# Performance work log

Measured on AMD Instinct MI355X. Metric: run time of the kernel, lower is better.

Reference implementation:

```python
import jax, jax.numpy as jnp
import numpy as np

B, N, D, H = 32, 512, 768, 12
HD = D // H  # 64
EPS = 1e-5


def layer_norm(x, g, b):
    mu = jnp.mean(x, axis=-1, keepdims=True)
    var = jnp.mean((x - mu) ** 2, axis=-1, keepdims=True)
    return (x - mu) / jnp.sqrt(var + EPS) * g + b


def setup_inputs() -> dict:
    key = jax.random.key(0)
    ks = jax.random.split(key, 10)
    x = jax.random.normal(ks[0], (B, N, D), dtype=jnp.float32)
    adj = jax.random.randint(ks[1], (B, N, N), 0, 2).astype(jnp.int32)
    adj = jnp.maximum(adj, jnp.eye(N, dtype=jnp.int32)[None])  # self-loops
    init = lambda k, shape: (jax.random.normal(k, shape, dtype=jnp.float32) * 0.02)
    return {
        "x": x, "adj": adj,
        "wq": init(ks[2], (D, D)), "bq": jnp.zeros((D,), jnp.float32),
        "wk": init(ks[3], (D, D)), "bk": jnp.zeros((D,), jnp.float32),
        "wv": init(ks[4], (D, D)), "bv": jnp.zeros((D,), jnp.float32),
        "wo": init(ks[5], (D, D)), "bo": jnp.zeros((D,), jnp.float32),
        "g1": jnp.ones((D,), jnp.float32), "b1": jnp.zeros((D,), jnp.float32),
        "g2": jnp.ones((D,), jnp.float32), "b2": jnp.zeros((D,), jnp.float32),
        "w_ffn1": init(ks[6], (D, 4 * D)), "b_ffn1": jnp.zeros((4 * D,), jnp.float32),
        "w_ffn2": init(ks[7], (4 * D, D)), "b_ffn2": jnp.zeros((D,), jnp.float32),
    }


def reference(x, adj, wq, bq, wk, bk, wv, bv, wo, bo, g1, b1, g2, b2,
              w_ffn1, b_ffn1, w_ffn2, b_ffn2):
    scale = HD ** -0.5
    h = layer_norm(x, g1, b1)
    split = lambda t: t.reshape(B, N, H, HD).transpose(0, 2, 1, 3)  # [B,H,N,HD]
    q = split(h @ wq + bq)
    k = split(h @ wk + bk)
    v = split(h @ wv + bv)
    scores = jnp.einsum('bhnd,bhmd->bhnm', q, k) * scale  # [B,H,N,N]
    scores = jnp.where(adj[:, None, :, :] == 0, -jnp.inf, scores)
    attn = jax.nn.softmax(scores, axis=-1)
    attn = jnp.nan_to_num(attn, nan=0.0)  # rows with no edges -> 0
    out = jnp.einsum('bhnm,bhmd->bhnd', attn, v)
    out = out.transpose(0, 2, 1, 3).reshape(B, N, D)
    out = out @ wo + bo + x  # residual (dropout=0, eval mode)
    h2 = layer_norm(out, g2, b2)
    ffn = jax.nn.gelu(h2 @ w_ffn1 + b_ffn1, approximate=False) @ w_ffn2 + b_ffn2
    return out + ffn
```

## Files before the change

kernel.cpp:

```cpp
#include <hip/hip_runtime.h>


#define Bn 32
#define Nn 512
#define Dn 768
#define Hn 12
#define HDn 64
#define Mn (Bn * Nn)
#define DFn 3072
#define MCHUNK 8192

typedef unsigned short u16;
typedef unsigned long long u64;
typedef short bf16x8 __attribute__((ext_vector_type(8)));
typedef float f32x4 __attribute__((ext_vector_type(4)));
typedef unsigned short u16x8 __attribute__((ext_vector_type(8)));

__device__ __forceinline__ float b2f(u16 u) {
    return __uint_as_float(((unsigned int)u) << 16);
}
__device__ __forceinline__ u16 f2b(float f) {
    unsigned int u = __float_as_uint(f);
    u += 0x7fffu + ((u >> 16) & 1u);
    return (u16)(u >> 16);
}
__device__ __forceinline__ float loadDyn(const void* p, size_t i, int f) {
    return f ? ((const float*)p)[i] : b2f(((const u16*)p)[i]);
}
__device__ __forceinline__ float gelu_exact(float x) {
    return 0.5f * x * (1.0f + erff(x * 0.70710678118654752f));
}

__device__ __forceinline__ void gl_lds16(const u16* g, u16* l) {
    __builtin_amdgcn_global_load_lds(
        (const __attribute__((address_space(1))) void*)(unsigned long long)(const void*)g,
        (__attribute__((address_space(3))) void*)(unsigned)(unsigned long long)(void*)l,
        16, 0, 0);
}

__global__ __launch_bounds__(256) void sniff_k(const u16* __restrict__ x,
                                               int* __restrict__ flag) {
    const int idx = blockIdx.x * 256 + threadIdx.x;
    u16x8 a = *(const u16x8*)&x[(size_t)idx * 8];
    int cnt = 0;
#pragma unroll
    for (int e = 0; e < 8; e++)
        cnt += ((a[e] & 0x7F80) == 0x7F80) ? 1 : 0;
#pragma unroll
    for (int off = 1; off <= 32; off <<= 1) cnt += __shfl_xor(cnt, off, 64);
    if ((threadIdx.x & 63) == 0 && cnt > 0) atomicAdd(flag, cnt);
}

__device__ __forceinline__ int flagval(const int* flagp) {
    return (*flagp > 32) ? 1 : 0;
}

__global__ __launch_bounds__(256) void pack_bias_k(
    const void* __restrict__ bq, const void* __restrict__ bk,
    const void* __restrict__ bv, const void* __restrict__ bo,
    const void* __restrict__ bf1, const void* __restrict__ bf2,
    float* __restrict__ out, const int* __restrict__ flagp) {
    const int f = flagval(flagp);
    const int i = blockIdx.x * 256 + threadIdx.x;
    if (i >= 6912) return;
    const void* src;
    int off;
    if (i < 768)       { src = bq;  off = i; }
    else if (i < 1536) { src = bk;  off = i - 768; }
    else if (i < 2304) { src = bv;  off = i - 1536; }
    else if (i < 3072) { src = bo;  off = i - 2304; }
    else if (i < 6144) { src = bf1; off = i - 3072; }
    else               { src = bf2; off = i - 6144; }
    out[i] = loadDyn(src, off, f);
}

__global__ __launch_bounds__(256) void mask_build_k(
    const int* __restrict__ adj, u64* __restrict__ mask) {
    const int idx = blockIdx.x * 256 + threadIdx.x;
    const size_t base = (size_t)(idx >> 3) * Nn + (size_t)(idx & 7) * 64;
    const int4* p = (const int4*)(adj + base);
    u64 m = 0;
#pragma unroll
    for (int c = 0; c < 16; c++) {
        int4 a = p[c];
        if (a.x) m |= 1ull << (c * 4 + 0);
        if (a.y) m |= 1ull << (c * 4 + 1);
        if (a.z) m |= 1ull << (c * 4 + 2);
        if (a.w) m |= 1ull << (c * 4 + 3);
    }
    mask[idx] = m;
}

__global__ __launch_bounds__(256) void transpose_k(
    const void* __restrict__ in, u16* __restrict__ out, int R, int C,
    const int* __restrict__ flagp) {
    const int f = flagval(flagp);
    __shared__ u16 tile[32][33];
    int c0 = blockIdx.x * 32, r0 = blockIdx.y * 32;
    int tx = threadIdx.x, ty = threadIdx.y;
#pragma unroll
    for (int i = 0; i < 32; i += 8)
        tile[ty + i][tx] = f2b(loadDyn(in, (size_t)(r0 + ty + i) * C + c0 + tx, f));
    __syncthreads();
#pragma unroll
    for (int i = 0; i < 32; i += 8)
        out[(size_t)(c0 + ty + i) * R + r0 + tx] = tile[tx][ty + i];
}

__global__ __launch_bounds__(256) void vtrans_k(
    const u16* __restrict__ v, u16* __restrict__ vt) {
    __shared__ u16 tile[32][33];
    const int bh = blockIdx.z;
    const int d0 = blockIdx.x * 32;
    const int n0 = blockIdx.y * 32;
    const int b = bh / Hn, h = bh % Hn;
    const int tx = threadIdx.x, ty = threadIdx.y;
#pragma unroll
    for (int i = 0; i < 32; i += 8)
        tile[ty + i][tx] =
            v[(size_t)(b * Nn + n0 + ty + i) * Dn + h * HDn + d0 + tx];
    __syncthreads();
#pragma unroll
    for (int i = 0; i < 32; i += 8)
        vt[((size_t)bh * HDn + d0 + ty + i) * Nn + n0 + tx] = tile[tx][ty + i];
}

template <int XDYN>
__global__ __launch_bounds__(256) void ln_k(
    const void* __restrict__ x, const void* __restrict__ g,
    const void* __restrict__ b, u16* __restrict__ y,
    const int* __restrict__ flagp) {
    const int f = flagval(flagp);
    const int t = threadIdx.x;
    const int row = blockIdx.x * 8 + (t >> 5);
    const int l32 = t & 31;
    const size_t base = (size_t)row * Dn;
    float v[24];
    if (XDYN == 0 || f == 0) {
        const u16* xp = (const u16*)x;
#pragma unroll
        for (int kk = 0; kk < 3; kk++) {
            u16x8 a = *(const u16x8*)&xp[base + kk * 256 + l32 * 8];
#pragma unroll
            for (int e = 0; e < 8; e++) v[kk * 8 + e] = b2f(a[e]);
        }
    } else {
#pragma unroll
        for (int kk = 0; kk < 3; kk++)
#pragma unroll
            for (int e = 0; e < 8; e++)
                v[kk * 8 + e] = loadDyn(x, base + kk * 256 + l32 * 8 + e, f);
    }
    float s = 0.f;
#pragma unroll
    for (int i = 0; i < 24; i++) s += v[i];
#pragma unroll
    for (int off = 1; off <= 16; off <<= 1) s += __shfl_xor(s, off, 64);
    const float mu = s * (1.0f / Dn);
    float d2 = 0.f;
#pragma unroll
    for (int i = 0; i < 24; i++) { float d = v[i] - mu; d2 += d * d; }
#pragma unroll
    for (int off = 1; off <= 16; off <<= 1) d2 += __shfl_xor(d2, off, 64);
    const float rstd = rsqrtf(d2 * (1.0f / Dn) + 1e-5f);
#pragma unroll
    for (int kk = 0; kk < 3; kk++) {
        const int c0 = kk * 256 + l32 * 8;
        u16x8 o;
        if (f == 0) {
            u16x8 gv = *(const u16x8*)&((const u16*)g)[c0];
            u16x8 bv = *(const u16x8*)&((const u16*)b)[c0];
#pragma unroll
            for (int e = 0; e < 8; e++)
                o[e] = f2b((v[kk * 8 + e] - mu) * rstd * b2f(gv[e]) + b2f(bv[e]));
        } else {
#pragma unroll
            for (int e = 0; e < 8; e++)
                o[e] = f2b((v[kk * 8 + e] - mu) * rstd * loadDyn(g, c0 + e, f)
                           + loadDyn(b, c0 + e, f));
        }
        *(u16x8*)&y[base + c0] = o;
    }
}

template <int ACT, int RES, int STORE, int WN, int CSPLIT>
__global__ __launch_bounds__(256, 3) void gemm_bt(
    const u16* __restrict__ A, const u16* __restrict__ Bt,
    const float* __restrict__ bias, const void* __restrict__ res,
    void* __restrict__ C, int M, int N, int K, int moff,
    const int* __restrict__ flagp) {
    constexpr int BN = 2 * WN;
    constexpr int NJ = WN / 16;
    constexpr int NB = BN / 64;
    const int f = flagval(flagp);
    __shared__ __align__(16) u16 As[2][128 * 32];
    __shared__ __align__(16) u16 Bs[2][BN * 32];
    const int tid = threadIdx.x;
    const int m0 = blockIdx.x * 128, n0 = blockIdx.y * BN;
    const int wave = tid >> 6, lane = tid & 63;
    const int wm = (wave & 1) * 64, wn = (wave >> 1) * WN;
    const int lm = lane & 15, quad = lane >> 4;

    const int koff = (tid & 3) * 8;
    const int srow = tid >> 2;
    const u16* gA[2];
    const u16* gB[NB];
#pragma unroll
    for (int i = 0; i < 2; i++)
        gA[i] = A + (size_t)(m0 + srow + i * 64) * K + koff;
#pragma unroll
    for (int i = 0; i < NB; i++)
        gB[i] = Bt + (size_t)(n0 + srow + i * 64) * K + koff;

    f32x4 acc[4][NJ] = {};

    auto stage = [&](int buf) {
#pragma unroll
        for (int i = 0; i < 2; i++) {
            gl_lds16(gA[i], &As[buf][(tid + i * 256) * 8]);
            gA[i] += 32;
        }
#pragma unroll
        for (int i = 0; i < NB; i++) {
            gl_lds16(gB[i], &Bs[buf][(tid + i * 256) * 8]);
            gB[i] += 32;
        }
    };
    auto compute = [&](int buf) {
        bf16x8 af[4], bfv[NJ];
#pragma unroll
        for (int i = 0; i < 4; i++)
            af[i] = *(const bf16x8*)&As[buf][(wm + i * 16 + lm) * 32 + quad * 8];
#pragma unroll
        for (int j = 0; j < NJ; j++)
            bfv[j] = *(const bf16x8*)&Bs[buf][(wn + j * 16 + lm) * 32 + quad * 8];
#pragma unroll
        for (int i = 0; i < 4; i++)
#pragma unroll
            for (int j = 0; j < NJ; j++)
                acc[i][j] = __builtin_amdgcn_mfma_f32_16x16x32_bf16(
                    af[i], bfv[j], acc[i][j], 0, 0, 0);
    };

    stage(0);
    int cur = 0;
    for (int k0 = 32; k0 < K; k0 += 32) {
        __syncthreads();
        stage(cur ^ 1);
        compute(cur);
        cur ^= 1;
    }
    __syncthreads();
    compute(cur);

    float bias_f[NJ];
#pragma unroll
    for (int j = 0; j < NJ; j++)
        bias_f[j] = bias[n0 + wn + j * 16 + lm];
#pragma unroll
    for (int i = 0; i < 4; i++) {
#pragma unroll
        for (int r = 0; r < 4; r++) {
            const int row = m0 + wm + i * 16 + quad * 4 + r;
#pragma unroll
            for (int j = 0; j < NJ; j++) {
                int col = n0 + wn + j * 16 + lm;
                size_t rb;
                if (CSPLIT > 0) {
                    const int reg = col / CSPLIT;
                    rb = ((size_t)reg * M + moff + row) * (size_t)CSPLIT;
                    col -= reg * CSPLIT;
                } else {
                    rb = (size_t)(moff + row) * N;
                }
                float vv = acc[i][j][r] + bias_f[j];
                if (ACT == 1) vv = gelu_exact(vv);
                if (RES == 1) vv += b2f(((const u16*)res)[rb + col]);
                if (RES == 2) vv += loadDyn(res, rb + col, f);
                if (STORE == 0) ((u16*)C)[rb + col] = f2b(vv);
                else {
                    if (f) ((float*)C)[rb + col] = vv;
                    else   ((u16*)C)[rb + col] = f2b(vv);
                }
            }
        }
    }
}

__global__ __launch_bounds__(256) void attn_mfma_k(
    const u16* q, const u16* __restrict__ k,
    const u16* __restrict__ vt, const u64* __restrict__ mask, u16* o) {
    const int h = blockIdx.x, qg = blockIdx.y, b = blockIdx.z;
    const int q0 = qg * 64;
    const int tid = threadIdx.x;
    const int wave = tid >> 6, lane = tid & 63;
    const int lm = lane & 15, quad = lane >> 4;
    const int wm = wave * 16;
    const int bh = b * Hn + h;
    const float SC2 = 0.125f * 1.4426950408889634f;

    __shared__ __align__(16) u16 Ks[64 * 72];
    __shared__ __align__(16) u16 Vts[64 * 72];
    __shared__ __align__(16) u16 Ps[64 * 72];

    const u16* qrow = q + ((size_t)(b * Nn + q0 + wm + lm)) * Dn + h * HDn + quad * 8;
    const bf16x8 aq0 = *(const bf16x8*)(qrow);
    const bf16x8 aq1 = *(const bf16x8*)(qrow + 32);

    const int srow = tid >> 2, scc = (tid & 3) * 16;
    const u16* kbase = k + ((size_t)(b * Nn + srow)) * Dn + h * HDn + scc;
    const u16* vbase = vt + ((size_t)bh * HDn + srow) * Nn + scc;

    u16x8 kr0 = *(const u16x8*)(kbase);
    u16x8 kr1 = *(const u16x8*)(kbase + 8);
    u16x8 vr0 = *(const u16x8*)(vbase);
    u16x8 vr1 = *(const u16x8*)(vbase + 8);

    float m_i[4], l_p[4];
#pragma unroll
    for (int r = 0; r < 4; r++) { m_i[r] = -3e38f; l_p[r] = 0.f; }
    f32x4 Oacc[4] = {};

    for (int kb = 0; kb < Nn / 64; kb++) {
        __syncthreads();
        *(u16x8*)&Ks[srow * 72 + scc]      = kr0;
        *(u16x8*)&Ks[srow * 72 + scc + 8]  = kr1;
        *(u16x8*)&Vts[srow * 72 + scc]     = vr0;
        *(u16x8*)&Vts[srow * 72 + scc + 8] = vr1;
        __syncthreads();
        if (kb + 1 < Nn / 64) {
            const u16* kn = kbase + (size_t)(kb + 1) * 64 * Dn;
            const u16* vn = vbase + (kb + 1) * 64;
            kr0 = *(const u16x8*)(kn);
            kr1 = *(const u16x8*)(kn + 8);
            vr0 = *(const u16x8*)(vn);
            vr1 = *(const u16x8*)(vn + 8);
        }
        f32x4 sacc[4] = {};
        __builtin_amdgcn_s_setprio(1);
#pragma unroll
        for (int s = 0; s < 2; s++) {
            const bf16x8 aq = s == 0 ? aq0 : aq1;
#pragma unroll
            for (int j = 0; j < 4; j++) {
                bf16x8 bk = *(const bf16x8*)&Ks[(j * 16 + lm) * 72 + s * 32 + quad * 8];
                sacc[j] = __builtin_amdgcn_mfma_f32_16x16x32_bf16(aq, bk, sacc[j], 0, 0, 0);
            }
        }
        __builtin_amdgcn_s_setprio(0);
        float alpha[4];
#pragma unroll
        for (int r = 0; r < 4; r++) {
            const u64 mrow = mask[(size_t)(b * Nn + q0 + wm + quad * 4 + r) * 8 + kb];
#pragma unroll
            for (int j = 0; j < 4; j++) {
                const int bit = (int)((mrow >> (j * 16 + lm)) & 1ull);
                sacc[j][r] = bit ? sacc[j][r] * SC2 : -3e38f;
            }
            float mx = fmaxf(fmaxf(sacc[0][r], sacc[1][r]),
                             fmaxf(sacc[2][r], sacc[3][r]));
            mx = fmaxf(mx, __shfl_xor(mx, 1, 64));
            mx = fmaxf(mx, __shfl_xor(mx, 2, 64));
            mx = fmaxf(mx, __shfl_xor(mx, 4, 64));
            mx = fmaxf(mx, __shfl_xor(mx, 8, 64));
            const float newm = fmaxf(m_i[r], mx);
            alpha[r] = exp2f(m_i[r] - newm);
            m_i[r] = newm;
            float s_ = 0.f;
#pragma unroll
            for (int j = 0; j < 4; j++) {
                const float sc = sacc[j][r];
                const float p = (sc > -1e30f) ? exp2f(sc - newm) : 0.f;
                sacc[j][r] = p;
                s_ += p;
            }
            l_p[r] = l_p[r] * alpha[r] + s_;
        }
#pragma unroll
        for (int r = 0; r < 4; r++)
#pragma unroll
            for (int j = 0; j < 4; j++)
                Ps[(wm + quad * 4 + r) * 72 + j * 16 + lm] = f2b(sacc[j][r]);
#pragma unroll
        for (int j = 0; j < 4; j++)
#pragma unroll
            for (int r = 0; r < 4; r++) Oacc[j][r] *= alpha[r];
        __builtin_amdgcn_s_setprio(1);
#pragma unroll
        for (int s = 0; s < 2; s++) {
            bf16x8 ap = *(const bf16x8*)&Ps[(wm + lm) * 72 + s * 32 + quad * 8];
#pragma unroll
            for (int j = 0; j < 4; j++) {
                bf16x8 bv = *(const bf16x8*)&Vts[(j * 16 + lm) * 72 + s * 32 + quad * 8];
                Oacc[j] = __builtin_amdgcn_mfma_f32_16x16x32_bf16(ap, bv, Oacc[j], 0, 0, 0);
            }
        }
        __builtin_amdgcn_s_setprio(0);
    }
    float inv[4];
#pragma unroll
    for (int r = 0; r < 4; r++) {
        float l = l_p[r];
        l += __shfl_xor(l, 1, 64);
        l += __shfl_xor(l, 2, 64);
        l += __shfl_xor(l, 4, 64);
        l += __shfl_xor(l, 8, 64);
        inv[r] = (l > 0.f) ? 1.0f / l : 0.f;
    }
#pragma unroll
    for (int r = 0; r < 4; r++) {
        const int row = q0 + wm + quad * 4 + r;
        u16* dst = o + ((size_t)(b * Nn + row)) * Dn + h * HDn;
#pragma unroll
        for (int j = 0; j < 4; j++)
            dst[j * 16 + lm] = f2b(Oacc[j][r] * inv[r]);
    }
}

extern "C" void kernel_launch(void* const* d_in, const int* in_sizes, int n_in,
                              void* d_out, int out_size, void* d_ws,
                              size_t ws_size, hipStream_t stream) {
    const void* x   = d_in[0];
    const int* adj  = (const int*)d_in[1];
    const void* wq  = d_in[2];
    const void* bq  = d_in[3];
    const void* wk  = d_in[4];
    const void* bk  = d_in[5];
    const void* wv  = d_in[6];
    const void* bv  = d_in[7];
    const void* wo  = d_in[8];
    const void* bo  = d_in[9];
    const void* g1  = d_in[10];
    const void* b1  = d_in[11];
    const void* g2  = d_in[12];
    const void* b2  = d_in[13];
    const void* w1  = d_in[14];
    const void* bf1 = d_in[15];
    const void* w2  = d_in[16];
    const void* bf2 = d_in[17];

    char* ws = (char*)d_ws;
    size_t off = 0;
    auto alloc = [&](size_t bytes) -> char* {
        char* p = ws + off;
        off += (bytes + 255) & ~(size_t)255;
        return p;
    };
    int* flag = (int*)alloc(4);
    u16* wqkvT = (u16*)alloc((size_t)3 * Dn * Dn * 2);
    u16* woT  = (u16*)alloc((size_t)Dn * Dn * 2);
    u16* w1T  = (u16*)alloc((size_t)Dn * DFn * 2);
    u16* w2T  = (u16*)alloc((size_t)Dn * DFn * 2);
    float* biasf = (float*)alloc(6912 * 4);
    u64* maskbuf = (u64*)alloc((size_t)Mn * 8 * 8);
    const size_t S = (size_t)Mn * Dn * 2;
    u16* Rh = (u16*)alloc(S);
    u16* Rq = (u16*)alloc(S);
    u16* Rk = (u16*)alloc(S);
    u16* Rv = (u16*)alloc(S);

    hipMemsetAsync(flag, 0, 4, stream);
    sniff_k<<<64, 256, 0, stream>>>((const u16*)x, flag);
    mask_build_k<<<Mn * 8 / 256, 256, 0, stream>>>(adj, maskbuf);
    pack_bias_k<<<27, 256, 0, stream>>>(bq, bk, bv, bo, bf1, bf2, biasf, flag);

    dim3 tb(32, 8);
    transpose_k<<<dim3(Dn / 32, Dn / 32), tb, 0, stream>>>(wq, wqkvT, Dn, Dn, flag);
    transpose_k<<<dim3(Dn / 32, Dn / 32), tb, 0, stream>>>(wk, wqkvT + (size_t)Dn * Dn, Dn, Dn, flag);
    transpose_k<<<dim3(Dn / 32, Dn / 32), tb, 0, stream>>>(wv, wqkvT + (size_t)2 * Dn * Dn, Dn, Dn, flag);
    transpose_k<<<dim3(Dn / 32, Dn / 32), tb, 0, stream>>>(wo, woT, Dn, Dn, flag);
    transpose_k<<<dim3(DFn / 32, Dn / 32), tb, 0, stream>>>(w1, w1T, Dn, DFn, flag);
    transpose_k<<<dim3(Dn / 32, DFn / 32), tb, 0, stream>>>(w2, w2T, DFn, Dn, flag);

    ln_k<1><<<Mn / 8, 256, 0, stream>>>(x, g1, b1, Rh, flag);

    gemm_bt<0, 0, 0, 64, Dn><<<dim3(Mn / 128, 3 * Dn / 128), 256, 0, stream>>>(
        Rh, wqkvT, biasf, nullptr, Rq, Mn, 3 * Dn, Dn, 0, flag);

    vtrans_k<<<dim3(HDn / 32, Nn / 32, Bn * Hn), tb, 0, stream>>>(Rv, Rh);

    attn_mfma_k<<<dim3(Hn, Nn / 64, Bn), 256, 0, stream>>>(Rq, Rk, Rh, maskbuf, Rq);

    gemm_bt<0, 2, 0, 64, 0><<<dim3(Mn / 128, Dn / 128), 256, 0, stream>>>(
        Rq, woT, biasf + 2304, x, Rv, Mn, Dn, Dn, 0, flag);

    ln_k<0><<<Mn / 8, 256, 0, stream>>>(Rv, g2, b2, Rh, flag);

    u16* hidden = Rq;
    for (int c = 0; c < Mn / MCHUNK; c++) {
        gemm_bt<1, 0, 0, 64, 0><<<dim3(MCHUNK / 128, DFn / 128), 256, 0, stream>>>(
            Rh + (size_t)c * MCHUNK * Dn, w1T, biasf + 3072, nullptr, hidden,
            MCHUNK, DFn, Dn, 0, flag);
        gemm_bt<0, 1, 1, 64, 0><<<dim3(MCHUNK / 128, Dn / 128), 256, 0, stream>>>(
            hidden, w2T, biasf + 6144, Rv, d_out, MCHUNK, Dn, DFn, c * MCHUNK, flag);
    }
}
```

Measured before the change: 689.4 us.

## Transpose attention MFMA so each lane owns one query row

```diff
diff --git a/kernel.cpp b/kernel.cpp
--- a/kernel.cpp
+++ b/kernel.cpp
@@ -11,10 +11,12 @@
 #define MCHUNK 8192
 
 typedef unsigned short u16;
+typedef unsigned int u32;
 typedef unsigned long long u64;
 typedef short bf16x8 __attribute__((ext_vector_type(8)));
 typedef float f32x4 __attribute__((ext_vector_type(4)));
 typedef unsigned short u16x8 __attribute__((ext_vector_type(8)));
+typedef unsigned int u32x2 __attribute__((ext_vector_type(2)));
 
 __device__ __forceinline__ float b2f(u16 u) {
     return __uint_as_float(((unsigned int)u) << 16);
@@ -29,6 +31,18 @@
 }
 __device__ __forceinline__ float gelu_exact(float x) {
     return 0.5f * x * (1.0f + erff(x * 0.70710678118654752f));
+}
+
+#if __has_builtin(__builtin_amdgcn_exp2f)
+#define EXP2F(x) __builtin_amdgcn_exp2f(x)
+#else
+#define EXP2F(x) __expf((x) * 0.6931471805599453f)
+#endif
+
+__device__ __forceinline__ u32 pk_bf16(float lo, float hi) {
+    u32 r;
+    asm("v_cvt_pk_bf16_f32 %0, %1, %2" : "=v"(r) : "v"(lo), "v"(hi));
+    return r;
 }
 
 __device__ __forceinline__ void gl_lds16(const u16* g, u16* l) {
@@ -287,7 +301,7 @@
     }
 }
 
-__global__ __launch_bounds__(256) void attn_mfma_k(
+__global__ __launch_bounds__(256, 4) void attn_mfma_k(
     const u16* q, const u16* __restrict__ k,
     const u16* __restrict__ vt, const u64* __restrict__ mask, u16* o) {
     const int h = blockIdx.x, qg = blockIdx.y, b = blockIdx.z;
@@ -301,7 +315,7 @@
 
     __shared__ __align__(16) u16 Ks[64 * 72];
     __shared__ __align__(16) u16 Vts[64 * 72];
-    __shared__ __align__(16) u16 Ps[64 * 72];
+    __shared__ __align__(16) u16 PsT[64 * 72];
 
     const u16* qrow = q + ((size_t)(b * Nn + q0 + wm + lm)) * Dn + h * HDn + quad * 8;
     const bf16x8 aq0 = *(const bf16x8*)(qrow);
@@ -316,9 +330,7 @@
     u16x8 vr0 = *(const u16x8*)(vbase);
     u16x8 vr1 = *(const u16x8*)(vbase + 8);
 
-    float m_i[4], l_p[4];
-#pragma unroll
-    for (int r = 0; r < 4; r++) { m_i[r] = -3e38f; l_p[r] = 0.f; }
+    float msc = 0.f, l_p = 0.f;
     f32x4 Oacc[4] = {};
 
     for (int kb = 0; kb < Nn / 64; kb++) {
@@ -343,77 +355,79 @@
             const bf16x8 aq = s == 0 ? aq0 : aq1;
 #pragma unroll
             for (int j = 0; j < 4; j++) {
-                bf16x8 bk = *(const bf16x8*)&Ks[(j * 16 + lm) * 72 + s * 32 + quad * 8];
-                sacc[j] = __builtin_amdgcn_mfma_f32_16x16x32_bf16(aq, bk, sacc[j], 0, 0, 0);
+                bf16x8 ak = *(const bf16x8*)&Ks[(j * 16 + lm) * 72 + s * 32 + quad * 8];
+                sacc[j] = __builtin_amdgcn_mfma_f32_16x16x32_bf16(ak, aq, sacc[j], 0, 0, 0);
             }
         }
         __builtin_amdgcn_s_setprio(0);
-        float alpha[4];
-#pragma unroll
-        for (int r = 0; r < 4; r++) {
-            const u64 mrow = mask[(size_t)(b * Nn + q0 + wm + quad * 4 + r) * 8 + kb];
+        const u64 mrow = mask[(size_t)(b * Nn + q0 + wm + lm) * 8 + kb];
+        const u32 wlo = ((u32)mrow) >> (quad * 4);
+        const u32 whi = ((u32)(mrow >> 32)) >> (quad * 4);
+#pragma unroll
+        for (int j = 0; j < 4; j++) {
+            const u32 w = (j < 2) ? wlo : whi;
+            const int sh = (j & 1) * 16;
+#pragma unroll
+            for (int r = 0; r < 4; r++)
+                sacc[j][r] = ((w >> (sh + r)) & 1u) ? sacc[j][r] : -3e38f;
+        }
+        float mx = fmaxf(fmaxf(sacc[0][0], sacc[0][1]), fmaxf(sacc[0][2], sacc[0][3]));
+#pragma unroll
+        for (int j = 1; j < 4; j++)
+            mx = fmaxf(mx, fmaxf(fmaxf(sacc[j][0], sacc[j][1]),
+                                 fmaxf(sacc[j][2], sacc[j][3])));
+        mx = fmaxf(mx, __shfl_xor(mx, 16, 64));
+        mx = fmaxf(mx, __shfl_xor(mx, 32, 64));
+        const float mn = fmaxf(msc, mx * SC2);
+        const float alpha = EXP2F(msc - mn);
+        msc = mn;
+        float sum = 0.f;
+#pragma unroll
+        for (int j = 0; j < 4; j++)
+#pragma unroll
+            for (int r = 0; r < 4; r++) {
+                const float p = EXP2F(fmaf(sacc[j][r], SC2, -mn));
+                sacc[j][r] = p;
+                sum += p;
+            }
+        l_p = l_p * alpha + sum;
+#pragma unroll
+        for (int j = 0; j < 4; j++)
+#pragma unroll
+            for (int r = 0; r < 4; r++) Oacc[j][r] *= alpha;
+        {
+            u16* prow = &PsT[(wm + lm) * 72];
 #pragma unroll
             for (int j = 0; j < 4; j++) {
-                const int bit = (int)((mrow >> (j * 16 + lm)) & 1ull);
-                sacc[j][r] = bit ? sacc[j][r] * SC2 : -3e38f;
+                u32x2 pk;
+                pk.x = pk_bf16(sacc[j][0], sacc[j][1]);
+                pk.y = pk_bf16(sacc[j][2], sacc[j][3]);
+                *(u32x2*)&prow[j * 16 + quad * 4] = pk;
             }
-            float mx = fmaxf(fmaxf(sacc[0][r], sacc[1][r]),
-                             fmaxf(sacc[2][r], sacc[3][r]));
-            mx = fmaxf(mx, __shfl_xor(mx, 1, 64));
-            mx = fmaxf(mx, __shfl_xor(mx, 2, 64));
-            mx = fmaxf(mx, __shfl_xor(mx, 4, 64));
-            mx = fmaxf(mx, __shfl_xor(mx, 8, 64));
-            const float newm = fmaxf(m_i[r], mx);
-            alpha[r] = exp2f(m_i[r] - newm);
-            m_i[r] = newm;
-            float s_ = 0.f;
+        }
+        __builtin_amdgcn_s_setprio(1);
+#pragma unroll
+        for (int s = 0; s < 2; s++) {
+            bf16x8 bp = *(const bf16x8*)&PsT[(wm + lm) * 72 + s * 32 + quad * 8];
 #pragma unroll
             for (int j = 0; j < 4; j++) {
-                const float sc = sacc[j][r];
-                const float p = (sc > -1e30f) ? exp2f(sc - newm) : 0.f;
-                sacc[j][r] = p;
-                s_ += p;
+                bf16x8 av = *(const bf16x8*)&Vts[(j * 16 + lm) * 72 + s * 32 + quad * 8];
+                Oacc[j] = __builtin_amdgcn_mfma_f32_16x16x32_bf16(av, bp, Oacc[j], 0, 0, 0);
             }
-            l_p[r] = l_p[r] * alpha[r] + s_;
-        }
-#pragma unroll
-        for (int r = 0; r < 4; r++)
-#pragma unroll
-            for (int j = 0; j < 4; j++)
-                Ps[(wm + quad * 4 + r) * 72 + j * 16 + lm] = f2b(sacc[j][r]);
-#pragma unroll
-        for (int j = 0; j < 4; j++)
-#pragma unroll
-            for (int r = 0; r < 4; r++) Oacc[j][r] *= alpha[r];
-        __builtin_amdgcn_s_setprio(1);
-#pragma unroll
-        for (int s = 0; s < 2; s++) {
-            bf16x8 ap = *(const bf16x8*)&Ps[(wm + lm) * 72 + s * 32 + quad * 8];
-#pragma unroll
-            for (int j = 0; j < 4; j++) {
-                bf16x8 bv = *(const bf16x8*)&Vts[(j * 16 + lm) * 72 + s * 32 + quad * 8];
-                Oacc[j] = __builtin_amdgcn_mfma_f32_16x16x32_bf16(ap, bv, Oacc[j], 0, 0, 0);
-            }
         }
         __builtin_amdgcn_s_setprio(0);
     }
-    float inv[4];
-#pragma unroll
-    for (int r = 0; r < 4; r++) {
-        float l = l_p[r];
-        l += __shfl_xor(l, 1, 64);
-        l += __shfl_xor(l, 2, 64);
-        l += __shfl_xor(l, 4, 64);
-        l += __shfl_xor(l, 8, 64);
-        inv[r] = (l > 0.f) ? 1.0f / l : 0.f;
-    }
-#pragma unroll
-    for (int r = 0; r < 4; r++) {
-        const int row = q0 + wm + quad * 4 + r;
-        u16* dst = o + ((size_t)(b * Nn + row)) * Dn + h * HDn;
-#pragma unroll
-        for (int j = 0; j < 4; j++)
-            dst[j * 16 + lm] = f2b(Oacc[j][r] * inv[r]);
+    float l = l_p;
+    l += __shfl_xor(l, 16, 64);
+    l += __shfl_xor(l, 32, 64);
+    const float inv = (l > 0.f) ? 1.0f / l : 0.f;
+    u16* dst = o + ((size_t)(b * Nn + q0 + wm + lm)) * Dn + h * HDn;
+#pragma unroll
+    for (int j = 0; j < 4; j++) {
+        u32x2 pk;
+        pk.x = pk_bf16(Oacc[j][0] * inv, Oacc[j][1] * inv);
+        pk.y = pk_bf16(Oacc[j][2] * inv, Oacc[j][3] * inv);
+        *(u32x2*)&dst[j * 16 + quad * 4] = pk;
     }
 }
 
```

Result: faster. 645.0 us (-6.4%).
